# Optimization experiments

Measured on AMD Instinct MI355X. Metric: run time of the kernel, lower is better.

The kernel has to match this reference:

```python
import jax, jax.numpy as jnp
import numpy as np

DIM = 2048
ORDER = 4
L_MAX = 2048
BATCH = 4  # must equal ORDER due to broadcast in the original module
SEQ = 2048


def setup_inputs() -> dict:
    key = jax.random.key(0)
    k1, k2 = jax.random.split(key)
    x = jax.random.normal(k1, (BATCH, DIM, SEQ), dtype=jnp.float32)
    kernel = jax.random.normal(k2, (ORDER, DIM, L_MAX), dtype=jnp.float32) * 0.02
    bias = jnp.zeros((DIM,), dtype=jnp.float32)
    return {"x": x, "kernel": kernel, "bias": bias}


def reference(x, kernel, bias):
    # x: (B, dim, L); kernel: (order, dim, l_max); B == order by broadcast
    seq_len = x.shape[-1]
    n = 2 * seq_len  # zero-padded FFT length for linear (causal) convolution
    x_fft = jnp.fft.rfft(x, n=n, axis=-1)            # (B, dim, n//2+1) complex
    kernel_fft = jnp.fft.rfft(kernel, n=n, axis=-1)  # (order, dim, n//2+1)
    y_fft = x_fft * kernel_fft                       # broadcast: B == order
    y = jnp.fft.irfft(y_fft, n=n, axis=-1)[:, :, :seq_len]
    return y + x + bias[None, :, None]
```

## Files before the change

kernel.cpp:

```cpp
#include <hip/hip_runtime.h>

typedef __attribute__((ext_vector_type(8)))  short short8;
typedef __attribute__((ext_vector_type(16))) float f32x16;
typedef unsigned int uint;

#define SEQ   2048
#define KB0   1024
#define KSTR  1048
#define ZB    (KB0 + 4 * KSTR)
#define LDSU  (ZB + 32)

__device__ inline uint pack2(float lo, float hi_) {
    uint ul = __float_as_uint(lo), uh = __float_as_uint(hi_);
    ul = (ul + 0x7fffu + ((ul >> 16) & 1u)) >> 16;
    uh = (uh + 0x7fffu + ((uh >> 16) & 1u)) >> 16;
    return (ul & 0xffffu) | (uh << 16);
}

__device__ inline int swz(int v) { return v ^ ((v >> 3) & 28); }

#define MFMA(A, B, C) __builtin_amdgcn_mfma_f32_32x32x16_bf16( \
    __builtin_bit_cast(short8, A), __builtin_bit_cast(short8, B), C, 0, 0, 0)

__global__ __launch_bounds__(64, 2)
void hyena_mfma(const float* __restrict__ x, const float* __restrict__ kern,
                const float* __restrict__ bias, float* __restrict__ out)
{
    __shared__ __align__(16) uint lds[LDSU];
    char* ldsb = (char*)lds;

    const int l  = threadIdx.x;
    const int n  = l & 31;
    const int hi = l >> 5;
    const int row = blockIdx.x;
    const size_t rb = (size_t)row * SEQ;
    const float bv = bias[row & 2047];

    #pragma unroll
    for (int it = 0; it < 8; ++it) {
        const int e = it * 256 + 4 * l;
        float4 v = *(const float4*)&x[rb + e];
        uint2 w; w.x = pack2(v.x, v.y); w.y = pack2(v.z, v.w);
        *(uint2*)&lds[swz(e >> 1)] = w;
    }

    #pragma unroll
    for (int it = 0; it < 4; ++it) {
        const int j = it * 512 + 8 * l;
        const float* kp0 = &kern[rb + (j == 2040 ? 0 : (2036 - j))];
        const float* kp1 = &kern[rb + (2040 - j)];
        float4 f0 = *(const float4*)kp0;
        float4 f1 = *(const float4*)kp1;
        float4 f2 = *(const float4*)(kp1 + 4);
        if (j == 2040) { f0.x = 0.f; f0.y = 0.f; f0.z = 0.f; f0.w = 0.f; }
        const float k0 = f2.w, k1 = f2.z, k2 = f2.y, k3 = f2.x;
        const float k4 = f1.w, k5 = f1.z, k6 = f1.y, k7 = f1.x;
        const float k8 = f0.w, k9 = f0.z, k10 = f0.y;
        const int m = j >> 1;
        uint4 w0 = {pack2(k0,k1), pack2(k2,k3), pack2(k4,k5), pack2(k6,k7)};
        uint4 w1 = {pack2(k1,k2), pack2(k3,k4), pack2(k5,k6), pack2(k7,k8)};
        uint4 w2 = {pack2(k2,k3), pack2(k4,k5), pack2(k6,k7), pack2(k8,k9)};
        uint4 w3 = {pack2(k3,k4), pack2(k5,k6), pack2(k7,k8), pack2(k9,k10)};
        *(uint4*)&lds[KB0 + m]            = w0;
        *(uint4*)&lds[KB0 + KSTR + m]     = w1;
        *(uint4*)&lds[KB0 + 2 * KSTR + m] = w2;
        *(uint4*)&lds[KB0 + 3 * KSTR + m] = w3;
    }
    if (l < 16) {
        lds[KB0 + 1024 + l]            = 0u;
        lds[KB0 + KSTR + 1024 + l]     = 0u;
        lds[KB0 + 2 * KSTR + 1024 + l] = 0u;
        lds[KB0 + 3 * KSTR + 1024 + l] = 0u;
    }
    if (l < 32) lds[ZB + l] = 0u;

    const int st00 = 2047 - n + 8 * hi;
    const int c    = st00 & 3;
    int kb = (KB0 + c * KSTR + ((st00 - c) >> 1)) * 4 - 2048;
    int ua = 16 * n + 4 * hi;
    const int zb0 = ZB * 4 + 16 * hi;

    f32x16 acc0 = {}, acc1a = {}, acc1b = {};

    #pragma unroll 2
    for (int r = 0; r < 32; ++r) {
        const int b0  = swz(ua) * 4;
        const int b0s = swz(ua + 8) * 4;
        const int b1  = swz(ua + 512) * 4;
        const int b1s = swz(ua + 520) * 4;
        const int va0  = (n >= r) ? b0  : zb0;
        const int va0s = (n >= r) ? b0s : (zb0 + 32);
        uint4 a00 = *(const uint4*)(ldsb + va0);
        uint4 a01 = *(const uint4*)(ldsb + va0s);
        uint4 a10 = *(const uint4*)(ldsb + b1);
        uint4 a11 = *(const uint4*)(ldsb + b1s);

        uint2 p0 = *(const uint2*)(ldsb + kb + 2048);
        uint2 p1 = *(const uint2*)(ldsb + kb + 2056);
        uint2 p2 = *(const uint2*)(ldsb + kb + 2080);
        uint2 p3 = *(const uint2*)(ldsb + kb + 2088);
        uint2 p4 = *(const uint2*)(ldsb + kb);
        uint2 p5 = *(const uint2*)(ldsb + kb + 8);
        uint2 p6 = *(const uint2*)(ldsb + kb + 32);
        uint2 p7 = *(const uint2*)(ldsb + kb + 40);
        uint4 b00 = {p0.x, p0.y, p1.x, p1.y};
        uint4 b01 = {p2.x, p2.y, p3.x, p3.y};
        uint4 b10 = {p4.x, p4.y, p5.x, p5.y};
        uint4 b11 = {p6.x, p6.y, p7.x, p7.y};

        acc0  = MFMA(a00, b00, acc0);
        acc1a = MFMA(a10, b00, acc1a);
        acc0  = MFMA(a01, b01, acc0);
        acc1a = MFMA(a11, b01, acc1a);
        acc1b = MFMA(a00, b10, acc1b);
        acc1b = MFMA(a01, b11, acc1b);

        ua -= 16;
        kb -= 64;
    }

    #pragma unroll
    for (int mt = 0; mt < 2; ++mt) {
        #pragma unroll
        for (int t = 0; t < 16; ++t) {
            const int rloc = (t & 3) + 8 * (t >> 2) + 4 * hi;
            const int p = mt * 32 + rloc;
            const uint w = lds[swz(16 * p + (n >> 1))];
            const float xr = __uint_as_float((n & 1) ? (w & 0xffff0000u) : (w << 16));
            const float av = mt ? (acc1a[t] + acc1b[t]) : acc0[t];
            out[rb + (size_t)p * 32 + n] = av + xr + bv;
        }
    }
}

extern "C" void kernel_launch(void* const* d_in, const int* in_sizes, int n_in,
                              void* d_out, int out_size, void* d_ws, size_t ws_size,
                              hipStream_t stream) {
    const float* x    = (const float*)d_in[0];
    const float* kern = (const float*)d_in[1];
    const float* bias = (const float*)d_in[2];
    float* out = (float*)d_out;

    hipLaunchKernelGGL(hyena_mfma, dim3(4 * 2048), dim3(64), 0, stream,
                       x, kern, bias, out);
}
```

Baseline: 67.66 us.

## Split each row's MFMA reduction across two waves with LDS partial-sum exchange

Each block now uses two wavefronts instead of one. Each wave handles half of the 32 reduction steps of the Toeplitz-style MFMA convolution. The partial accumulators are then exchanged through LDS so that each wave finalises one 32-row output tile. Global loads for x and the kernel are spread over 128 threads. This halves the serial MFMA chain per wave and raises latency hiding, at the cost of added __syncthreads barriers, an LDS exchange of partial sums, and a possible occupancy change under the new launch bounds.

```diff
diff --git a/kernel.cpp b/kernel.cpp
--- a/kernel.cpp
+++ b/kernel.cpp
@@ -9,6 +9,8 @@
 #define KSTR  1048
 #define ZB    (KB0 + 4 * KSTR)
 #define LDSU  (ZB + 32)
+#define EX0   KB0
+#define EX1   (KB0 + 1344)
 
 __device__ inline uint pack2(float lo, float hi_) {
     uint ul = __float_as_uint(lo), uh = __float_as_uint(hi_);
@@ -22,31 +24,33 @@
 #define MFMA(A, B, C) __builtin_amdgcn_mfma_f32_32x32x16_bf16( \
     __builtin_bit_cast(short8, A), __builtin_bit_cast(short8, B), C, 0, 0, 0)
 
-__global__ __launch_bounds__(64, 2)
+__global__ __launch_bounds__(128, 3)
 void hyena_mfma(const float* __restrict__ x, const float* __restrict__ kern,
                 const float* __restrict__ bias, float* __restrict__ out)
 {
     __shared__ __align__(16) uint lds[LDSU];
     char* ldsb = (char*)lds;
 
-    const int l  = threadIdx.x;
-    const int n  = l & 31;
-    const int hi = l >> 5;
+    const int tid = threadIdx.x;
+    const int wv  = tid >> 6;
+    const int l   = tid & 63;
+    const int n   = l & 31;
+    const int hi  = l >> 5;
     const int row = blockIdx.x;
     const size_t rb = (size_t)row * SEQ;
     const float bv = bias[row & 2047];
 
     #pragma unroll
-    for (int it = 0; it < 8; ++it) {
-        const int e = it * 256 + 4 * l;
+    for (int it = 0; it < 4; ++it) {
+        const int e = it * 512 + 4 * tid;
         float4 v = *(const float4*)&x[rb + e];
-        uint2 w; w.x = pack2(v.x, v.y); w.y = pack2(v.z, v.w);
-        *(uint2*)&lds[swz(e >> 1)] = w;
+        uint2 w2; w2.x = pack2(v.x, v.y); w2.y = pack2(v.z, v.w);
+        *(uint2*)&lds[swz(e >> 1)] = w2;
     }
 
     #pragma unroll
-    for (int it = 0; it < 4; ++it) {
-        const int j = it * 512 + 8 * l;
+    for (int it = 0; it < 2; ++it) {
+        const int j = it * 1024 + 8 * tid;
         const float* kp0 = &kern[rb + (j == 2040 ? 0 : (2036 - j))];
         const float* kp1 = &kern[rb + (2040 - j)];
         float4 f0 = *(const float4*)kp0;
@@ -66,24 +70,27 @@
         *(uint4*)&lds[KB0 + 2 * KSTR + m] = w2;
         *(uint4*)&lds[KB0 + 3 * KSTR + m] = w3;
     }
-    if (l < 16) {
-        lds[KB0 + 1024 + l]            = 0u;
-        lds[KB0 + KSTR + 1024 + l]     = 0u;
-        lds[KB0 + 2 * KSTR + 1024 + l] = 0u;
-        lds[KB0 + 3 * KSTR + 1024 + l] = 0u;
+    if (tid < 16) {
+        lds[KB0 + 1024 + tid]            = 0u;
+        lds[KB0 + KSTR + 1024 + tid]     = 0u;
+        lds[KB0 + 2 * KSTR + 1024 + tid] = 0u;
+        lds[KB0 + 3 * KSTR + 1024 + tid] = 0u;
     }
-    if (l < 32) lds[ZB + l] = 0u;
+    if (tid < 32) lds[ZB + tid] = 0u;
+    __syncthreads();
 
+    const int R0   = wv << 4;
     const int st00 = 2047 - n + 8 * hi;
     const int c    = st00 & 3;
-    int kb = (KB0 + c * KSTR + ((st00 - c) >> 1)) * 4 - 2048;
-    int ua = 16 * n + 4 * hi;
+    int kb = (KB0 + c * KSTR + ((st00 - c) >> 1)) * 4 - 2048 - (R0 << 6);
+    int ua = 16 * n + 4 * hi - (R0 << 4);
     const int zb0 = ZB * 4 + 16 * hi;
 
     f32x16 acc0 = {}, acc1a = {}, acc1b = {};
 
     #pragma unroll 2
-    for (int r = 0; r < 32; ++r) {
+    for (int i = 0; i < 16; ++i) {
+        const int r = R0 + i;
         const int b0  = swz(ua) * 4;
         const int b0s = swz(ua + 8) * 4;
         const int b1  = swz(ua + 512) * 4;
@@ -118,18 +125,33 @@
         ua -= 16;
         kb -= 64;
     }
+    __syncthreads();
+
+    f32x16 part_send, part_keep;
+    if (wv == 0) { part_send = acc1a + acc1b; part_keep = acc0; }
+    else         { part_send = acc0;          part_keep = acc1a + acc1b; }
+    const int exw = (wv == 0) ? EX0 : EX1;
+    const int exr = (wv == 0) ? EX1 : EX0;
+    #pragma unroll
+    for (int q = 0; q < 4; ++q) {
+        float4 f = {part_send[4*q], part_send[4*q+1], part_send[4*q+2], part_send[4*q+3]};
+        *(float4*)(ldsb + 4 * (exw + l * 20) + 16 * q) = f;
+    }
+    __syncthreads();
+    f32x16 tile = part_keep;
+    #pragma unroll
+    for (int q = 0; q < 4; ++q) {
+        float4 f = *(const float4*)(ldsb + 4 * (exr + l * 20) + 16 * q);
+        tile[4*q] += f.x; tile[4*q+1] += f.y; tile[4*q+2] += f.z; tile[4*q+3] += f.w;
+    }
 
     #pragma unroll
-    for (int mt = 0; mt < 2; ++mt) {
-        #pragma unroll
-        for (int t = 0; t < 16; ++t) {
-            const int rloc = (t & 3) + 8 * (t >> 2) + 4 * hi;
-            const int p = mt * 32 + rloc;
-            const uint w = lds[swz(16 * p + (n >> 1))];
-            const float xr = __uint_as_float((n & 1) ? (w & 0xffff0000u) : (w << 16));
-            const float av = mt ? (acc1a[t] + acc1b[t]) : acc0[t];
-            out[rb + (size_t)p * 32 + n] = av + xr + bv;
-        }
+    for (int t = 0; t < 16; ++t) {
+        const int rloc = (t & 3) + 8 * (t >> 2) + 4 * hi;
+        const int p = 32 * wv + rloc;
+        const uint w = lds[swz(16 * p + (n >> 1))];
+        const float xr = __uint_as_float((n & 1) ? (w & 0xffff0000u) : (w << 16));
+        out[rb + (size_t)p * 32 + n] = tile[t] + xr + bv;
     }
 }
 
@@ -141,6 +163,6 @@
     const float* bias = (const float*)d_in[2];
     float* out = (float*)d_out;
 
-    hipLaunchKernelGGL(hyena_mfma, dim3(4 * 2048), dim3(64), 0, stream,
+    hipLaunchKernelGGL(hyena_mfma, dim3(4 * 2048), dim3(128), 0, stream,
                        x, kern, bias, out);
 }
```

Measured after the change: 60.63 us. -10.4%, faster.
